# Kernel tuning notes

Hardware: AMD Instinct MI355X
Metric: run time of the kernel (lower is better)

The kernel has to match this reference:

```python
import jax, jax.numpy as jnp
import numpy as np

H = 16; KV = 4; D = 128; HID = 2048; MAX_POS = 4096; RANK = 8; ALPHA = 16.0; THETA = 10000.0


def _lora_dense(x, kernel, a, b):
    # base kernel path is stop-gradient'd in the original LoRADense
    x = x.astype(jnp.bfloat16)
    y = x @ jax.lax.stop_gradient(kernel.astype(jnp.bfloat16))
    y = y + (ALPHA / RANK) * ((x @ a.astype(jnp.bfloat16)) @ b.astype(jnp.bfloat16))
    return y.astype(jnp.float32)


def _apply_rope(xq, xk, position_ids):
    # complex rotation expressed with real cos/sin on interleaved (even, odd) pairs
    dt = xq.dtype
    xq = xq.astype(jnp.bfloat16).astype(jnp.float32)
    xk = xk.astype(jnp.bfloat16).astype(jnp.float32)
    d = xq.shape[-1]
    inv_freq = 1.0 / THETA ** (jnp.arange(0, d, 2)[: d // 2].astype(jnp.float32) / d)
    angles = jnp.arange(MAX_POS, dtype=jnp.float32)[:, None] * inv_freq[None, :]  # (max_pos, d/2)
    cos = jnp.cos(angles)[position_ids][:, :, None, :]  # (b, s, 1, d/2)
    sin = jnp.sin(angles)[position_ids][:, :, None, :]

    def rot(x):
        xe = x[..., 0::2]
        xo = x[..., 1::2]
        re = xe * cos - xo * sin
        im = xe * sin + xo * cos
        return jnp.stack((re, im), axis=-1).reshape(x.shape)

    return rot(xq).astype(dt), rot(xk).astype(dt)


def _forward(hidden_states, attention_mask, position_ids, wq_kernel, wq_a, wq_b,
             wk_kernel, wk_a, wk_b, wv_kernel, wv_a, wv_b, wo_kernel, wo_a, wo_b):
    b, s, _ = hidden_states.shape
    hs = hidden_states.astype(jnp.bfloat16)
    xq = _lora_dense(hs, wq_kernel, wq_a, wq_b).reshape(b, s, H, D)
    g = H // KV
    # GQA: repeat each kv head g times along the head axis ('b s (h d) -> b s (h g) d')
    xk = jnp.repeat(_lora_dense(hs, wk_kernel, wk_a, wk_b).reshape(b, s, KV, D), g, axis=2)
    xv = jnp.repeat(_lora_dense(hs, wv_kernel, wv_a, wv_b).reshape(b, s, KV, D), g, axis=2)
    xq, xk = _apply_rope(xq, xk, position_ids)
    causal = jnp.tril(jnp.ones((s, s), dtype=bool))
    mask = attention_mask[:, None, None, :] & causal[None, None]  # (b, 1, q, k)
    bias = jnp.where(mask, 0.0, jnp.finfo(jnp.float32).min)
    scale = 1.0 / np.sqrt(D).astype(np.float32)
    scores = jnp.einsum('bqhd,bkhd->bhqk', (xq * scale).astype(jnp.bfloat16),
                        xk.astype(jnp.bfloat16)).astype(jnp.float32) + bias
    attn = jax.nn.softmax(scores, axis=-1)
    out = jnp.einsum('bhqk,bkhd->bqhd', attn, xv).reshape(b, s, H * D)
    return _lora_dense(out, wo_kernel, wo_a, wo_b)


def setup_inputs():
    key = jax.random.key(0)
    ks = jax.random.split(key, 16)
    B, S = 2, 2048
    w = lambda k, shp, sc=0.02: jax.random.normal(k, shp, dtype=jnp.float32) * sc
    return {
        'hidden_states': jax.random.normal(ks[0], (B, S, HID), dtype=jnp.float32),
        'attention_mask': jnp.ones((B, S), dtype=bool),
        'position_ids': jnp.broadcast_to(jnp.arange(S, dtype=jnp.int32), (B, S)),
        'wq_kernel': w(ks[1], (HID, H * D)),
        'wq_a': w(ks[2], (HID, RANK), 0.01),
        'wq_b': w(ks[3], (RANK, H * D), 0.01),
        'wk_kernel': w(ks[4], (HID, KV * D)),
        'wk_a': w(ks[5], (HID, RANK), 0.01),
        'wk_b': w(ks[6], (RANK, KV * D), 0.01),
        'wv_kernel': w(ks[7], (HID, KV * D)),
        'wv_a': w(ks[8], (HID, RANK), 0.01),
        'wv_b': w(ks[9], (RANK, KV * D), 0.01),
        'wo_kernel': w(ks[10], (H * D, HID)),
        'wo_a': w(ks[11], (H * D, RANK), 0.01),
        'wo_b': w(ks[12], (RANK, HID), 0.01),
    }


def reference(hidden_states, attention_mask, position_ids, wq_kernel, wq_a, wq_b,
              wk_kernel, wk_a, wk_b, wv_kernel, wv_a, wv_b, wo_kernel, wo_a, wo_b):
    return _forward(hidden_states, attention_mask, position_ids, wq_kernel, wq_a, wq_b,
                    wk_kernel, wk_a, wk_b, wv_kernel, wv_a, wv_b, wo_kernel, wo_a, wo_b)
```

## Files before the change

### kernel.cpp

```cpp
#include <hip/hip_runtime.h>
#include <hip/hip_bf16.h>
#include <cstdint>

#define H_    16
#define KV_   4
#define D_    128
#define HID_  2048
#define B_    2
#define S_    2048
#define NROW_ (B_*S_)
#define HD_   (H_*D_)
#define KVD_  (KV_*D_)
#define NQKV_ (HD_ + 2*KVD_)
#define SCALE_ 0.08838834764831843f
#define NEG_  -1e30f

typedef float  f32x4  __attribute__((ext_vector_type(4)));
typedef __bf16 bf16x8 __attribute__((ext_vector_type(8)));
typedef __bf16 bf16x4 __attribute__((ext_vector_type(4)));

__device__ __forceinline__ unsigned short f2bf(float x) {
  unsigned u = __float_as_uint(x);
  return (unsigned short)((u + 0x7FFFu + ((u >> 16) & 1u)) >> 16);
}
__device__ __forceinline__ float bf2f(unsigned short h) {
  return __uint_as_float(((unsigned)h) << 16);
}

__device__ __forceinline__ void glds16(const void* g, void* l) {
  typedef __attribute__((address_space(1))) const char G;
  typedef __attribute__((address_space(3))) char L;
  __builtin_amdgcn_global_load_lds((const G*)(unsigned long long)g,
                                   (L*)(unsigned)(unsigned long long)l, 16, 0, 0);
}

__global__ __launch_bounds__(256) void fold_w2(const float* __restrict__ W,
                                               const float* __restrict__ A,
                                               const float* __restrict__ Bm,
                                               unsigned short* __restrict__ Wt,
                                               int K, int N) {
  __shared__ float Bs[8 * 64];
  __shared__ unsigned short tt[64 * 72];
  const int tid = threadIdx.x;
  const int k0 = blockIdx.x << 6, n0 = blockIdx.y << 6;
#pragma unroll
  for (int i = 0; i < 2; ++i) {
    int c = i * 256 + tid;
    Bs[c] = bf2f(f2bf(Bm[(c >> 6) * N + n0 + (c & 63)]));
  }
  __syncthreads();
  const int kr = tid >> 2, nc = (tid & 3) << 4;
  float a[8];
#pragma unroll
  for (int r = 0; r < 8; ++r) a[r] = 2.0f * bf2f(f2bf(A[(k0 + kr) * 8 + r]));
#pragma unroll
  for (int i = 0; i < 4; ++i) {
    float4 wv = *(const float4*)(W + (size_t)(k0 + kr) * N + n0 + nc + i * 4);
    float e[4] = {wv.x, wv.y, wv.z, wv.w};
#pragma unroll
    for (int q = 0; q < 4; ++q) {
      int n = nc + i * 4 + q;
      float acc = bf2f(f2bf(e[q]));
#pragma unroll
      for (int r = 0; r < 8; ++r) acc += a[r] * Bs[r * 64 + n];
      tt[kr * 72 + n] = f2bf(acc);
    }
  }
  __syncthreads();
  const int nr = tid >> 2, kc = (tid & 3) << 4;
#pragma unroll
  for (int i = 0; i < 2; ++i) {
    unsigned short o[8];
#pragma unroll
    for (int e2 = 0; e2 < 8; ++e2) o[e2] = tt[(kc + i * 8 + e2) * 72 + nr];
    *(bf16x8*)(Wt + (size_t)(n0 + nr) * K + k0 + kc + i * 8) = *(const bf16x8*)o;
  }
}

__global__ __launch_bounds__(256) void cast_x(const float* __restrict__ in,
                                              unsigned short* __restrict__ out, int n4) {
  int i = blockIdx.x * 256 + threadIdx.x;
  if (i >= n4) return;
  float4 v = ((const float4*)in)[i];
  ushort4 o; o.x = f2bf(v.x); o.y = f2bf(v.y); o.z = f2bf(v.z); o.w = f2bf(v.w);
  ((ushort4*)out)[i] = o;
}

__global__ void trig_k(float* __restrict__ tab) {
  int p = blockIdx.x, j = threadIdx.x;
  float invf = __powf(10000.0f, -(float)j / 64.0f);
  float a = (float)p * invf;
  float s, c;
  sincosf(a, &s, &c);
  tab[(p * 64 + j) * 2 + 0] = c;
  tab[(p * 64 + j) * 2 + 1] = s;
}

__global__ __launch_bounds__(256) void rope2(unsigned short* __restrict__ QKV,
                                             const int* __restrict__ pos,
                                             const float* __restrict__ trig) {
  int gid = blockIdx.x * 256 + threadIdx.x;
  int row = gid / 160;
  int ch = gid - row * 160;
  bool isq = ch < 128;
  int col = isq ? (ch << 4) : (HD_ + ((ch - 128) << 4));
  int j0 = (isq ? (ch & 7) : ((ch - 128) & 7)) << 3;
  int pp = pos[row];
  const float* tb = trig + ((size_t)pp * 64 + j0) * 2;
  float4 t0 = *(const float4*)(tb);
  float4 t1 = *(const float4*)(tb + 4);
  float4 t2 = *(const float4*)(tb + 8);
  float4 t3 = *(const float4*)(tb + 12);
  float cc[8] = {t0.x, t0.z, t1.x, t1.z, t2.x, t2.z, t3.x, t3.z};
  float ss[8] = {t0.y, t0.w, t1.y, t1.w, t2.y, t2.w, t3.y, t3.w};
  unsigned short* base = QKV + (size_t)row * NQKV_ + col;
  unsigned short xin[16], xo[16];
  *(bf16x8*)xin = *(const bf16x8*)base;
  *(bf16x8*)(xin + 8) = *(const bf16x8*)(base + 8);
  float scl = isq ? SCALE_ : 1.0f;
#pragma unroll
  for (int p = 0; p < 8; ++p) {
    float x0 = bf2f(xin[2 * p]), x1 = bf2f(xin[2 * p + 1]);
    float re = (x0 * cc[p] - x1 * ss[p]) * scl;
    float im = (x0 * ss[p] + x1 * cc[p]) * scl;
    xo[2 * p] = f2bf(re); xo[2 * p + 1] = f2bf(im);
  }
  *(bf16x8*)base = *(const bf16x8*)xo;
  *(bf16x8*)(base + 8) = *(const bf16x8*)(xo + 8);
}

__global__ __launch_bounds__(256) void vtrans_k(const unsigned short* __restrict__ QKV,
                                                unsigned short* __restrict__ VT) {
  __shared__ unsigned short t[64 * 65];
  const int tid = threadIdx.x;
  const int s0 = blockIdx.x << 6, d0 = blockIdx.y << 6;
  const int bk = blockIdx.z, b = bk >> 2, hkv = bk & 3;
#pragma unroll
  for (int i = 0; i < 2; ++i) {
    int c = i * 256 + tid;
    int sr = c >> 3, c8 = c & 7;
    bf16x8 v = *(const bf16x8*)(QKV + (size_t)(b * S_ + s0 + sr) * NQKV_
                                + HD_ + KVD_ + hkv * D_ + d0 + c8 * 8);
    const unsigned short* u = (const unsigned short*)&v;
#pragma unroll
    for (int k = 0; k < 8; ++k) t[sr * 65 + c8 * 8 + k] = u[k];
  }
  __syncthreads();
#pragma unroll
  for (int i = 0; i < 2; ++i) {
    int c = i * 256 + tid;
    int dr = c >> 3, c8 = c & 7;
    unsigned short o[8];
#pragma unroll
    for (int k = 0; k < 8; ++k) o[k] = t[(c8 * 8 + k) * 65 + dr];
    *(bf16x8*)(VT + ((size_t)(bk * 128 + d0 + dr)) * S_ + s0 + c8 * 8) =
        *(const bf16x8*)o;
  }
}

template <int BN, int OUTF32>
__global__ __launch_bounds__(512, 1) void gemm256(const unsigned short* __restrict__ A,
                                                  const unsigned short* __restrict__ Bt,
                                                  void* __restrict__ C,
                                                  int M, int N, int K) {
  constexpr int ASLAB = 256 * 32;
  constexpr int BSLAB = BN * 32;
  constexpr int BUFE = 2 * ASLAB + 2 * BSLAB;
  constexpr int NFR = BN / 64;
  constexpr int WCOL = BN / 4;
  constexpr int BCHUNK = BN / 16;
  __shared__ __align__(16) unsigned short lds[2 * BUFE];
  const int tid = threadIdx.x, lane = tid & 63, w = tid >> 6;
  const int g = lane >> 4, l15 = lane & 15;
  const int wm = w >> 2, wn = w & 3;

  const int x = blockIdx.x & 7, inner = blockIdx.x >> 3;
  const int bm = (x >> 1) * 4 + (inner >> 3);
  const int bn = (x & 1) * 8 + (inner & 7);
  const int row0 = bm << 8, col0 = bn * BN;

  auto stageA = [&](int kt, int kh, int buf) {
#pragma unroll
    for (int i = 0; i < 2; ++i) {
      int ci = i * 8 + w;
      int L = ci * 64 + lane;
      int r = L >> 2, c = L & 3;
      int sc = c ^ ((r >> 1) & 3);
      glds16(A + (size_t)(row0 + r) * K + (kt << 6) + kh * 32 + sc * 8,
             (char*)lds + (size_t)(buf * BUFE + kh * ASLAB) * 2 + (size_t)ci * 1024);
    }
  };
  auto stageB = [&](int kt, int kh, int buf) {
#pragma unroll
    for (int i = 0; i < (BCHUNK + 7) / 8; ++i) {
      int ci = i * 8 + w;
      if (ci < BCHUNK) {
        int L = ci * 64 + lane;
        int r = L >> 2, c = L & 3;
        int sc = c ^ ((r >> 1) & 3);
        glds16(Bt + (size_t)(col0 + r) * K + (kt << 6) + kh * 32 + sc * 8,
               (char*)lds + (size_t)(buf * BUFE + 2 * ASLAB + kh * BSLAB) * 2 + (size_t)ci * 1024);
      }
    }
  };
  auto waitG = [&]() {
    if constexpr (BCHUNK > 8) {
      if (w < BCHUNK - 8) asm volatile("s_waitcnt vmcnt(4)" ::: "memory");
      else                asm volatile("s_waitcnt vmcnt(3)" ::: "memory");
    } else {
      asm volatile("s_waitcnt vmcnt(3)" ::: "memory");
    }
  };

  f32x4 acc[8][NFR];
#pragma unroll
  for (int i = 0; i < 8; ++i)
#pragma unroll
    for (int j = 0; j < NFR; ++j) acc[i][j] = (f32x4){0.f, 0.f, 0.f, 0.f};

  bf16x8 af[4], bfr[NFR];
  auto rdA = [&](int buf, int kh, int mh) {
#pragma unroll
    for (int mi = 0; mi < 4; ++mi) {
      int r = wm * 128 + mh * 64 + mi * 16 + l15;
      int cc = g ^ ((r >> 1) & 3);
      af[mi] = *(const bf16x8*)(lds + buf * BUFE + kh * ASLAB + r * 32 + cc * 8);
    }
  };
  auto rdB = [&](int buf, int kh) {
#pragma unroll
    for (int ni = 0; ni < NFR; ++ni) {
      int r = wn * WCOL + ni * 16 + l15;
      int cc = g ^ ((r >> 1) & 3);
      bfr[ni] = *(const bf16x8*)(lds + buf * BUFE + 2 * ASLAB + kh * BSLAB + r * 32 + cc * 8);
    }
  };
  auto domfma = [&](int mh) {
    __builtin_amdgcn_s_setprio(1);
#pragma unroll
    for (int mi = 0; mi < 4; ++mi)
#pragma unroll
      for (int ni = 0; ni < NFR; ++ni)
        acc[mh * 4 + mi][ni] =
            __builtin_amdgcn_mfma_f32_16x16x32_bf16(af[mi], bfr[ni], acc[mh * 4 + mi][ni], 0, 0, 0);
    __builtin_amdgcn_s_setprio(0);
  };

  stageA(0, 0, 0); stageB(0, 0, 0); stageA(0, 1, 0); stageB(0, 1, 0);
  asm volatile("s_waitcnt vmcnt(0)" ::: "memory");
  __builtin_amdgcn_s_barrier();

  const int nkt = K >> 6;
  for (int kt = 0; kt < nkt; ++kt) {
    const int buf = kt & 1, nb = buf ^ 1;
    const bool more = kt + 1 < nkt;
    if (more) stageA(kt + 1, 0, nb);
    rdA(buf, 0, 0); rdB(buf, 0);
    __builtin_amdgcn_s_barrier();
    domfma(0);
    __builtin_amdgcn_s_barrier();
    if (more) { stageB(kt + 1, 0, nb); waitG(); }
    else      { asm volatile("s_waitcnt vmcnt(0)" ::: "memory"); }
    rdA(buf, 0, 1);
    __builtin_amdgcn_s_barrier();
    domfma(1);
    __builtin_amdgcn_s_barrier();
    if (more) stageA(kt + 1, 1, nb);
    rdA(buf, 1, 0); rdB(buf, 1);
    __builtin_amdgcn_s_barrier();
    domfma(0);
    __builtin_amdgcn_s_barrier();
    if (more) { stageB(kt + 1, 1, nb); waitG(); }
    rdA(buf, 1, 1);
    __builtin_amdgcn_s_barrier();
    domfma(1);
    __builtin_amdgcn_s_barrier();
  }

#pragma unroll
  for (int mi8 = 0; mi8 < 8; ++mi8)
#pragma unroll
    for (int jj = 0; jj < 4; ++jj) {
      int r = row0 + wm * 128 + mi8 * 16 + g * 4 + jj;
#pragma unroll
      for (int ni = 0; ni < NFR; ++ni) {
        int cc = col0 + wn * WCOL + ni * 16 + l15;
        float v = acc[mi8][ni][jj];
        if (OUTF32) ((float*)C)[(size_t)r * N + cc] = v;
        else        ((unsigned short*)C)[(size_t)r * N + cc] = f2bf(v);
      }
    }
}

__global__ __launch_bounds__(256) void attn_k(const unsigned short* __restrict__ QKV,
                                              const unsigned short* __restrict__ VT,
                                              unsigned short* __restrict__ O) {
  __shared__ __align__(16) unsigned short smem[37376];
  const int tid = threadIdx.x, lane = tid & 63, w = tid >> 6;
  const int g = lane >> 4, l15 = lane & 15;

  const int dd = blockIdx.x;
  const int grp = dd & 7;
  const int t64 = dd >> 3;
  const int pair = t64 & 15;
  const int bh = grp * 4 + (t64 >> 4);
  const int b = bh >> 4, h = bh & 15, hkv = (h >> 2);

  const unsigned short* QKVk0 = QKV + (size_t)b * S_ * NQKV_ + HD_ + hkv * D_;
  const unsigned short* VT0  = VT + (size_t)(b * 4 + hkv) * 128 * S_;

  int gk[4], gv[4], dsl[4];
#pragma unroll
  for (int i = 0; i < 4; ++i) {
    int c = i * 256 + w * 64 + lane;
    { int r = c >> 4, s = c & 15; gk[i] = r * NQKV_ + (s ^ (r & 7)) * 8; }
    { int d = c >> 3, s = c & 7;  gv[i] = d * S_ + (s ^ (d & 7)) * 8; }
    dsl[i] = (i * 256 + w * 64) * 16;
  }
  int koff[4][4], voff[2][8], pwo[4], pro[2];
#pragma unroll
  for (int ks = 0; ks < 4; ++ks)
#pragma unroll
    for (int m = 0; m < 4; ++m) {
      int r = m * 16 + l15;
      koff[ks][m] = r * 128 + ((ks * 4 + g) ^ (r & 7)) * 8;
    }
#pragma unroll
  for (int ks = 0; ks < 2; ++ks)
#pragma unroll
    for (int nd = 0; nd < 8; ++nd) {
      int d = nd * 16 + l15;
      voff[ks][nd] = d * 64 + ((ks * 4 + g) ^ (d & 7)) * 8;
    }
#pragma unroll
  for (int m = 0; m < 4; ++m) pwo[m] = l15 * 72 + m * 16 + g * 4;
#pragma unroll
  for (int ks = 0; ks < 2; ++ks) pro[ks] = l15 * 72 + ks * 32 + g * 8;
  const int PB = 32768 + w * 1152;
  char* const smemc = (char*)smem;

#define STAGE(KB, KOB, VOB) do {                                            \
    const unsigned short* bk_ = QKVk0 + (size_t)(KB) * NQKV_;               \
    const unsigned short* bv_ = VT0 + (KB);                                 \
    _Pragma("unroll")                                                       \
    for (int i_ = 0; i_ < 4; ++i_) {                                        \
      glds16(bk_ + gk[i_], smemc + (KOB) + dsl[i_]);                        \
      glds16(bv_ + gv[i_], smemc + (VOB) + dsl[i_]);                        \
    }                                                                       \
  } while (0)

#define COMPUTE(KOH, VOH, TCUR) do {                                        \
    f32x4 sacc[4];                                                          \
    _Pragma("unroll") for (int m = 0; m < 4; ++m)                           \
      sacc[m] = (f32x4){0.f, 0.f, 0.f, 0.f};                                \
    __builtin_amdgcn_s_setprio(1);                                          \
    _Pragma("unroll") for (int ks = 0; ks < 4; ++ks) {                      \
      bf16x8 kf[4];                                                         \
      _Pragma("unroll") for (int m = 0; m < 4; ++m)                         \
        kf[m] = *(const bf16x8*)(smem + (KOH) + koff[ks][m]);               \
      _Pragma("unroll") for (int m = 0; m < 4; ++m)                         \
        sacc[m] = __builtin_amdgcn_mfma_f32_16x16x32_bf16(kf[m], qf[ks], sacc[m], 0, 0, 0); \
    }                                                                       \
    __builtin_amdgcn_s_setprio(0);                                          \
    if ((TCUR) == qt) {                                                     \
      _Pragma("unroll") for (int m = 0; m < 4; ++m)                         \
        _Pragma("unroll") for (int jj = 0; jj < 4; ++jj)                    \
          if (m * 16 + g * 4 + jj > w * 16 + l15) sacc[m][jj] = NEG_;       \
    }                                                                       \
    float pm = NEG_;                                                        \
    _Pragma("unroll") for (int m = 0; m < 4; ++m)                           \
      _Pragma("unroll") for (int jj = 0; jj < 4; ++jj)                      \
        pm = fmaxf(pm, sacc[m][jj]);                                        \
    pm = fmaxf(pm, __shfl_xor(pm, 16));                                     \
    pm = fmaxf(pm, __shfl_xor(pm, 32));                                     \
    bool skip = __all(pm <= mrun + 8.f);                                    \
    float mnew = skip ? mrun : fmaxf(mrun, pm);                             \
    float ls = 0.f;                                                         \
    _Pragma("unroll") for (int m = 0; m < 4; ++m)                           \
      _Pragma("unroll") for (int jj = 0; jj < 4; ++jj) {                    \
        float pv = __expf(sacc[m][jj] - mnew);                              \
        sacc[m][jj] = pv;                                                   \
        ls += pv;                                                           \
      }                                                                     \
    ls += __shfl_xor(ls, 16);                                               \
    ls += __shfl_xor(ls, 32);                                               \
    if (skip) {                                                             \
      lrun += ls;                                                           \
    } else {                                                                \
      float sc = __expf(mrun - mnew);                                       \
      lrun = lrun * sc + ls;                                                \
      mrun = mnew;                                                          \
      _Pragma("unroll") for (int jj = 0; jj < 4; ++jj) {                    \
        int srcl = (lane & 48) | (g * 4 + jj);                              \
        float s = __shfl(sc, srcl);                                         \
        _Pragma("unroll") for (int nd = 0; nd < 8; ++nd) oacc[nd][jj] *= s; \
      }                                                                     \
    }                                                                       \
    _Pragma("unroll") for (int m = 0; m < 4; ++m) {                         \
      bf16x4 pk = {(__bf16)sacc[m][0], (__bf16)sacc[m][1],                  \
                   (__bf16)sacc[m][2], (__bf16)sacc[m][3]};                 \
      *(bf16x4*)(smem + PB + pwo[m]) = pk;                                  \
    }                                                                       \
    __builtin_amdgcn_s_setprio(1);                                          \
    _Pragma("unroll") for (int ks = 0; ks < 2; ++ks) {                      \
      bf16x8 pf = *(const bf16x8*)(smem + PB + pro[ks]);                    \
      _Pragma("unroll") for (int nd = 0; nd < 8; ++nd) {                    \
        bf16x8 vf = *(const bf16x8*)(smem + (VOH) + voff[ks][nd]);          \
        oacc[nd] = __builtin_amdgcn_mfma_f32_16x16x32_bf16(pf, vf, oacc[nd], 0, 0, 0); \
      }                                                                     \
    }                                                                       \
    __builtin_amdgcn_s_setprio(0);                                          \
  } while (0)

  for (int qsel = 0; qsel < 2; ++qsel) {
    const int qt = qsel ? (31 - pair) : pair;
    const int q_base = qt << 6;
    const int ntile = qt + 1;

    bf16x8 qf[4];
#pragma unroll
    for (int ks = 0; ks < 4; ++ks)
      qf[ks] = *(const bf16x8*)(QKV + (size_t)(b * S_ + q_base + w * 16 + l15) * NQKV_
                                + h * D_ + ks * 32 + g * 8);

    f32x4 oacc[8];
#pragma unroll
    for (int nd = 0; nd < 8; ++nd) oacc[nd] = (f32x4){0.f, 0.f, 0.f, 0.f};
    float mrun = NEG_, lrun = 0.f;

    STAGE(0, 0, 32768);
    __syncthreads();
    for (int t = 0; t < ntile; t += 2) {
      const bool m1 = t + 1 < ntile;
      if (m1) STAGE((t + 1) << 6, 16384, 49152);
      COMPUTE(0, 16384, t);
      __syncthreads();
      if (!m1) break;
      if (t + 2 < ntile) STAGE((t + 2) << 6, 0, 32768);
      COMPUTE(8192, 24576, t + 1);
      __syncthreads();
    }

    float inv[4];
#pragma unroll
    for (int jj = 0; jj < 4; ++jj) {
      int srcl = (lane & 48) | (g * 4 + jj);
      inv[jj] = 1.0f / __shfl(lrun, srcl);
    }
    unsigned short* sE = smem;
#pragma unroll
    for (int nd = 0; nd < 8; ++nd)
#pragma unroll
      for (int jj = 0; jj < 4; ++jj) {
        __bf16 e = (__bf16)(oacc[nd][jj] * inv[jj]);
        sE[(w * 16 + g * 4 + jj) * 136 + nd * 16 + l15] = *(unsigned short*)&e;
      }
    __syncthreads();
#pragma unroll
    for (int i = 0; i < 4; ++i) {
      int c = i * 256 + tid;
      int r = c >> 4, c16 = c & 15;
      bf16x8 vv = *(const bf16x8*)(sE + r * 136 + c16 * 8);
      *(bf16x8*)(O + (size_t)(b * S_ + q_base + r) * HD_ + h * D_ + c16 * 8) = vv;
    }
    __syncthreads();
  }
#undef STAGE
#undef COMPUTE
}

extern "C" void kernel_launch(void* const* d_in, const int* in_sizes, int n_in,
                              void* d_out, int out_size, void* d_ws, size_t ws_size,
                              hipStream_t stream) {
  const float* hs  = (const float*)d_in[0];
  const int*   pos = (const int*)d_in[2];
  const float* wq  = (const float*)d_in[3];
  const float* wqa = (const float*)d_in[4];
  const float* wqb = (const float*)d_in[5];
  const float* wk  = (const float*)d_in[6];
  const float* wka = (const float*)d_in[7];
  const float* wkb = (const float*)d_in[8];
  const float* wv  = (const float*)d_in[9];
  const float* wva = (const float*)d_in[10];
  const float* wvb = (const float*)d_in[11];
  const float* wo  = (const float*)d_in[12];
  const float* woa = (const float*)d_in[13];
  const float* wob = (const float*)d_in[14];

  char* ws = (char*)d_ws;
  unsigned short* Xb   = (unsigned short*)(ws);
  unsigned short* Wqkv = (unsigned short*)(ws + 16777216);
  unsigned short* Wot  = (unsigned short*)(ws + 29360128);
  unsigned short* QKV  = (unsigned short*)(ws + 37748736);
  unsigned short* VT   = (unsigned short*)(ws + 62914560);
  float*          trig = (float*)(ws + 67108864);

  fold_w2<<<dim3(32, 32), 256, 0, stream>>>(wq, wqa, wqb, Wqkv, 2048, 2048);
  fold_w2<<<dim3(32, 8),  256, 0, stream>>>(wk, wka, wkb, Wqkv + (size_t)2048 * 2048, 2048, 512);
  fold_w2<<<dim3(32, 8),  256, 0, stream>>>(wv, wva, wvb, Wqkv + (size_t)2560 * 2048, 2048, 512);
  fold_w2<<<dim3(32, 32), 256, 0, stream>>>(wo, woa, wob, Wot, 2048, 2048);
  cast_x<<<8192, 256, 0, stream>>>(hs, Xb, 2097152);
  trig_k<<<2048, 64, 0, stream>>>(trig);
  gemm256<192, 0><<<256, 512, 0, stream>>>(Xb, Wqkv, QKV, 4096, 3072, 2048);
  rope2<<<2560, 256, 0, stream>>>(QKV, pos, trig);
  vtrans_k<<<dim3(32, 2, 8), 256, 0, stream>>>(QKV, VT);
  attn_k<<<512, 256, 0, stream>>>(QKV, VT, Xb );
  gemm256<128, 1><<<256, 512, 0, stream>>>(Xb, Wot, d_out, 4096, 2048, 2048);
}
```

Before: 209.4 us.

## Fuse Q rotary embedding into attention and switch softmax to exp2

The rotary embedding for Q now runs inside the attention kernel when Q fragments are loaded, with log2(e) folded into the Q scale. The standalone rope kernel therefore only handles K, which cuts its launch size and the Q read-modify-write traffic through QKV. Softmax uses the hardware exp2 builtin with a rescaled skip threshold. The cross-lane row-sum reduction moves out of the per-tile loop to the end, and the P store to shared memory is placed earlier. This adds trig-table loads and some ALU work to the attention prologue.

```diff
diff --git a/kernel.cpp b/kernel.cpp
--- a/kernel.cpp
+++ b/kernel.cpp
@@ -13,6 +13,9 @@
 #define KVD_  (KV_*D_)
 #define NQKV_ (HD_ + 2*KVD_)
 #define SCALE_ 0.08838834764831843f
+#define L2E_   1.44269504088896f
+#define QSC_   (SCALE_ * L2E_)
+#define THR2_  11.5415603f
 #define NEG_  -1e30f
 
 typedef float  f32x4  __attribute__((ext_vector_type(4)));
@@ -96,15 +99,14 @@
   tab[(p * 64 + j) * 2 + 1] = s;
 }
 
-__global__ __launch_bounds__(256) void rope2(unsigned short* __restrict__ QKV,
+__global__ __launch_bounds__(256) void ropeK(unsigned short* __restrict__ QKV,
                                              const int* __restrict__ pos,
                                              const float* __restrict__ trig) {
   int gid = blockIdx.x * 256 + threadIdx.x;
-  int row = gid / 160;
-  int ch = gid - row * 160;
-  bool isq = ch < 128;
-  int col = isq ? (ch << 4) : (HD_ + ((ch - 128) << 4));
-  int j0 = (isq ? (ch & 7) : ((ch - 128) & 7)) << 3;
+  int row = gid >> 5;
+  int ch = gid & 31;
+  int col = HD_ + (ch << 4);
+  int j0 = (ch & 7) << 3;
   int pp = pos[row];
   const float* tb = trig + ((size_t)pp * 64 + j0) * 2;
   float4 t0 = *(const float4*)(tb);
@@ -117,13 +119,11 @@
   unsigned short xin[16], xo[16];
   *(bf16x8*)xin = *(const bf16x8*)base;
   *(bf16x8*)(xin + 8) = *(const bf16x8*)(base + 8);
-  float scl = isq ? SCALE_ : 1.0f;
 #pragma unroll
   for (int p = 0; p < 8; ++p) {
     float x0 = bf2f(xin[2 * p]), x1 = bf2f(xin[2 * p + 1]);
-    float re = (x0 * cc[p] - x1 * ss[p]) * scl;
-    float im = (x0 * ss[p] + x1 * cc[p]) * scl;
-    xo[2 * p] = f2bf(re); xo[2 * p + 1] = f2bf(im);
+    xo[2 * p]     = f2bf(x0 * cc[p] - x1 * ss[p]);
+    xo[2 * p + 1] = f2bf(x0 * ss[p] + x1 * cc[p]);
   }
   *(bf16x8*)base = *(const bf16x8*)xo;
   *(bf16x8*)(base + 8) = *(const bf16x8*)(xo + 8);
@@ -294,7 +294,9 @@
 
 __global__ __launch_bounds__(256) void attn_k(const unsigned short* __restrict__ QKV,
                                               const unsigned short* __restrict__ VT,
-                                              unsigned short* __restrict__ O) {
+                                              unsigned short* __restrict__ O,
+                                              const int* __restrict__ pos,
+                                              const float* __restrict__ trig) {
   __shared__ __align__(16) unsigned short smem[37376];
   const int tid = threadIdx.x, lane = tid & 63, w = tid >> 6;
   const int g = lane >> 4, l15 = lane & 15;
@@ -373,21 +375,24 @@
         pm = fmaxf(pm, sacc[m][jj]);                                        \
     pm = fmaxf(pm, __shfl_xor(pm, 16));                                     \
     pm = fmaxf(pm, __shfl_xor(pm, 32));                                     \
-    bool skip = __all(pm <= mrun + 8.f);                                    \
+    bool skip = __all(pm <= mrun + THR2_);                                  \
     float mnew = skip ? mrun : fmaxf(mrun, pm);                             \
     float ls = 0.f;                                                         \
     _Pragma("unroll") for (int m = 0; m < 4; ++m)                           \
       _Pragma("unroll") for (int jj = 0; jj < 4; ++jj) {                    \
-        float pv = __expf(sacc[m][jj] - mnew);                              \
+        float pv = __builtin_amdgcn_exp2f(sacc[m][jj] - mnew);              \
         sacc[m][jj] = pv;                                                   \
         ls += pv;                                                           \
       }                                                                     \
-    ls += __shfl_xor(ls, 16);                                               \
-    ls += __shfl_xor(ls, 32);                                               \
+    _Pragma("unroll") for (int m = 0; m < 4; ++m) {                         \
+      bf16x4 pk = {(__bf16)sacc[m][0], (__bf16)sacc[m][1],                  \
+                   (__bf16)sacc[m][2], (__bf16)sacc[m][3]};                 \
+      *(bf16x4*)(smem + PB + pwo[m]) = pk;                                  \
+    }                                                                       \
     if (skip) {                                                             \
       lrun += ls;                                                           \
     } else {                                                                \
-      float sc = __expf(mrun - mnew);                                       \
+      float sc = __builtin_amdgcn_exp2f(mrun - mnew);                       \
       lrun = lrun * sc + ls;                                                \
       mrun = mnew;                                                          \
       _Pragma("unroll") for (int jj = 0; jj < 4; ++jj) {                    \
@@ -395,11 +400,6 @@
         float s = __shfl(sc, srcl);                                         \
         _Pragma("unroll") for (int nd = 0; nd < 8; ++nd) oacc[nd][jj] *= s; \
       }                                                                     \
-    }                                                                       \
-    _Pragma("unroll") for (int m = 0; m < 4; ++m) {                         \
-      bf16x4 pk = {(__bf16)sacc[m][0], (__bf16)sacc[m][1],                  \
-                   (__bf16)sacc[m][2], (__bf16)sacc[m][3]};                 \
-      *(bf16x4*)(smem + PB + pwo[m]) = pk;                                  \
     }                                                                       \
     __builtin_amdgcn_s_setprio(1);                                          \
     _Pragma("unroll") for (int ks = 0; ks < 2; ++ks) {                      \
@@ -417,11 +417,29 @@
     const int q_base = qt << 6;
     const int ntile = qt + 1;
 
+    const int qrow = q_base + w * 16 + l15;
+    const int pp = pos[b * S_ + qrow];
+    const float* trow = trig + (size_t)pp * 128;
     bf16x8 qf[4];
 #pragma unroll
-    for (int ks = 0; ks < 4; ++ks)
-      qf[ks] = *(const bf16x8*)(QKV + (size_t)(b * S_ + q_base + w * 16 + l15) * NQKV_
-                                + h * D_ + ks * 32 + g * 8);
+    for (int ks = 0; ks < 4; ++ks) {
+      bf16x8 raw = *(const bf16x8*)(QKV + (size_t)(b * S_ + qrow) * NQKV_
+                                    + h * D_ + ks * 32 + g * 8);
+      const float* tb = trow + (ks * 16 + g * 4) * 2;
+      float4 t01 = *(const float4*)(tb);
+      float4 t23 = *(const float4*)(tb + 4);
+      float cc4[4] = {t01.x, t01.z, t23.x, t23.z};
+      float ss4[4] = {t01.y, t01.w, t23.y, t23.w};
+      const unsigned short* ru = (const unsigned short*)&raw;
+      unsigned short qo[8];
+#pragma unroll
+      for (int p2 = 0; p2 < 4; ++p2) {
+        float x0 = bf2f(ru[2 * p2]), x1 = bf2f(ru[2 * p2 + 1]);
+        qo[2 * p2]     = f2bf((x0 * cc4[p2] - x1 * ss4[p2]) * QSC_);
+        qo[2 * p2 + 1] = f2bf((x0 * ss4[p2] + x1 * cc4[p2]) * QSC_);
+      }
+      qf[ks] = *(const bf16x8*)qo;
+    }
 
     f32x4 oacc[8];
 #pragma unroll
@@ -440,6 +458,9 @@
       COMPUTE(8192, 24576, t + 1);
       __syncthreads();
     }
+
+    lrun += __shfl_xor(lrun, 16);
+    lrun += __shfl_xor(lrun, 32);
 
     float inv[4];
 #pragma unroll
@@ -502,8 +523,8 @@
   cast_x<<<8192, 256, 0, stream>>>(hs, Xb, 2097152);
   trig_k<<<2048, 64, 0, stream>>>(trig);
   gemm256<192, 0><<<256, 512, 0, stream>>>(Xb, Wqkv, QKV, 4096, 3072, 2048);
-  rope2<<<2560, 256, 0, stream>>>(QKV, pos, trig);
+  ropeK<<<512, 256, 0, stream>>>(QKV, pos, trig);
   vtrans_k<<<dim3(32, 2, 8), 256, 0, stream>>>(QKV, VT);
-  attn_k<<<512, 256, 0, stream>>>(QKV, VT, Xb );
+  attn_k<<<512, 256, 0, stream>>>(QKV, VT, Xb , pos, trig);
   gemm256<128, 1><<<256, 512, 0, stream>>>(Xb, Wot, d_out, 4096, 2048, 2048);
 }
```

Result: slower. 231.5 us (+10.5%).
